# Performance work log

Measured on AMD Instinct MI355X. Metric: run time of the kernel, lower is better.

Reference implementation:

```python
import jax, jax.numpy as jnp
import numpy as np

B, F_IN, F_OUT, D, K = 32, 64, 64, 512, 64


def setup_inputs() -> dict:
    key = jax.random.key(0)
    k1, k2, k3 = jax.random.split(key, 3)
    x = jax.random.normal(k1, (B, F_IN, D), dtype=jnp.float32)
    # Evaluated monomial-word operators: K matrices of size D x D
    word_ops = jax.random.normal(k2, (K, D, D), dtype=jnp.float32)
    # nn.init.uniform_ -> U[0,1)
    coeff = jax.random.uniform(k3, (F_OUT, F_IN, K), dtype=jnp.float32)
    return {"x": x, "word_ops": word_ops, "coeff": coeff}


def reference(x, word_ops, coeff):
    # Per sample in the torch code:
    #   evals[i, d, k] = (X @ W_k)[i, d] = sum_e X[i, e] * W[k, e, d]
    #   res = tensordot(coeff, evals, ([1, 2], [0, 2]))  -> [F_out, D]
    # Fully batched fused contraction (replaces the Python loop over batch):
    # evals: [B, F_in, D, K]
    evals = jnp.einsum('bie,ked->bidk', x, word_ops)
    # out: [B, F_out, D]
    out = jnp.einsum('oik,bidk->bod', coeff, evals)
    return out
```

## Files before the change

kernel.cpp:

```cpp
#include <hip/hip_runtime.h>
#include <hip/hip_bf16.h>


#define KK 32768

typedef __attribute__((ext_vector_type(8))) short bf16x8;
typedef __attribute__((ext_vector_type(4))) float f32x4;

__device__ __forceinline__ unsigned short f2bf(float f) {
  unsigned int u = __float_as_uint(f);
  return (unsigned short)((u + 0x7FFFu + ((u >> 16) & 1u)) >> 16);
}

__device__ __forceinline__ unsigned int pkbf2(float a, float b) {
  __hip_bfloat162 h = __float22bfloat162_rn(make_float2(a, b));
  return *(unsigned int*)&h;
}

__device__ __forceinline__ void gld16(void* lds, const void* g) {
  __builtin_amdgcn_global_load_lds((const __attribute__((address_space(1))) void*)g,
                                   (__attribute__((address_space(3))) void*)lds,
                                   16, 0, 0);
}

__global__ __launch_bounds__(256) void convW(const float* __restrict__ W,
                                             unsigned short* __restrict__ WbT) {
  __shared__ float tile[64][65];
  int bx = blockIdx.x;
  int k = bx >> 6, et = (bx >> 3) & 7, dt = bx & 7;
  int t = threadIdx.x;
  const float* src = W + ((size_t)k * 512 + (size_t)et * 64) * 512 + dt * 64;
  int rr = t >> 6, cc = t & 63;
#pragma unroll
  for (int p = 0; p < 16; p++) {
    int e = p * 4 + rr;
    tile[e][cc] = src[(size_t)e * 512 + cc];
  }
  __syncthreads();
  int dl = t >> 4, eg = t & 15;
#pragma unroll
  for (int p = 0; p < 4; p++) {
    int d = p * 16 + dl;
    ushort4 v;
    v.x = f2bf(tile[eg * 4 + 0][d]);
    v.y = f2bf(tile[eg * 4 + 1][d]);
    v.z = f2bf(tile[eg * 4 + 2][d]);
    v.w = f2bf(tile[eg * 4 + 3][d]);
    *(ushort4*)(WbT + (size_t)(dt * 64 + d) * KK + k * 512 + et * 64 + eg * 4) = v;
  }
}

__global__ __launch_bounds__(256) void convXC(const float* __restrict__ x,
                                              const float* __restrict__ c,
                                              unsigned short* __restrict__ xT,
                                              unsigned short* __restrict__ cb) {
  __shared__ unsigned short lds[64 * 130];
  int t = threadIdx.x;
  if (blockIdx.x < 128) {
    int bx = blockIdx.x;
    int b = bx >> 2, ec = bx & 3;
    const float* src = x + (size_t)b * 32768 + ec * 128;
#pragma unroll
    for (int j = 0; j < 32; j++) {
      int idx = j * 256 + t;
      int i = idx >> 7, e = idx & 127;
      lds[i * 130 + e] = f2bf(src[(size_t)i * 512 + e]);
    }
    __syncthreads();
    unsigned short* dst = xT + (size_t)b * 32768 + ec * 128 * 64;
#pragma unroll
    for (int j = 0; j < 32; j++) {
      int idx = j * 256 + t;
      int e = idx >> 6, i = idx & 63;
      dst[idx] = lds[i * 130 + e];
    }
  } else {
    int rb = blockIdx.x - 128;
    const float* src = c + (size_t)rb * 4096;
#pragma unroll
    for (int j = 0; j < 16; j++) {
      int idx = j * 256 + t;
      int r = idx >> 6, k = idx & 63;
      lds[r * 66 + k] = f2bf(src[idx]);
    }
    __syncthreads();
#pragma unroll
    for (int j = 0; j < 16; j++) {
      int idx = j * 256 + t;
      int k = idx >> 6, r = idx & 63;
      cb[(size_t)k * 4096 + rb * 64 + r] = lds[r * 66 + k];
    }
  }
}

__global__ __launch_bounds__(256, 2) void fused_kern(const unsigned short* __restrict__ xT,
                                                     const unsigned short* __restrict__ cb,
                                                     const unsigned short* __restrict__ Bt,
                                                     float* __restrict__ out) {
  __shared__ unsigned short u[128 * 64];
  __shared__ unsigned short Bs[256 * 64];
  __shared__ unsigned short ck[4 * 64 * 64];
  int bx = blockIdx.x;
  int ks = bx & 15, np = (bx >> 4) & 1, mt = bx >> 5;
  int m0 = mt * 128, n0 = np * 256, kw0 = ks * 4, b0 = mt * 2;
  int t = threadIdx.x;
  int wid = t >> 6, lane = t & 63, q = lane >> 4, l16 = lane & 15;
  int wmb = wid & 1;
  int wnh = wid >> 1;
  int srow = t >> 3;
  int cg = (t & 7) ^ (srow & 7);
  {
    const unsigned short* gc = cb + (size_t)kw0 * 4096;
#pragma unroll
    for (int j = 0; j < 8; j++) {
      int row = j * 32 + srow;
      gld16((char*)ck + (j * 256 + t) * 16, gc + (size_t)row * 64 + cg * 8);
    }
  }
  f32x4 acc[4][8] = {};
#pragma unroll 1
  for (int ec = 0; ec < 8; ec++) {
#pragma unroll
    for (int j = 0; j < 4; j++) {
      int row = j * 32 + srow;
      int bl = row >> 6, el = row & 63;
      gld16((char*)u + (j * 256 + t) * 16,
            xT + (size_t)(b0 + bl) * 32768 + (size_t)(ec * 64 + el) * 64 + cg * 8);
    }
    __syncthreads();
    bf16x8 ax[4][2];
#pragma unroll
    for (int et = 0; et < 4; et++)
#pragma unroll
      for (int ks2 = 0; ks2 < 2; ks2++) {
        int row = wmb * 64 + et * 16 + l16;
        int s2 = (ks2 * 4 + q) ^ (row & 7);
        ax[et][ks2] = *(const bf16x8*)(u + row * 64 + s2 * 8);
      }
    __syncthreads();
#pragma unroll 1
    for (int k = 0; k < 4; k++) {
      const unsigned short* gb = Bt + (size_t)n0 * KK + (size_t)(kw0 + k) * 512 + ec * 64;
#pragma unroll
      for (int j = 0; j < 8; j++) {
        int row = j * 32 + srow;
        gld16((char*)Bs + (j * 256 + t) * 16, gb + (size_t)row * KK + cg * 8);
      }
      const unsigned short* ckk = ck + k * 4096;
      bf16x8 bc[2][2];
#pragma unroll
      for (int otl = 0; otl < 2; otl++)
#pragma unroll
        for (int ks2 = 0; ks2 < 2; ks2++) {
          int o = (wnh * 2 + otl) * 16 + l16;
          int s2 = (ks2 * 4 + q) ^ (o & 7);
          bc[otl][ks2] = *(const bf16x8*)(ckk + o * 64 + s2 * 8);
        }
      f32x4 td[4][2] = {};
#pragma unroll
      for (int et = 0; et < 4; et++)
#pragma unroll
        for (int otl = 0; otl < 2; otl++)
#pragma unroll
          for (int ks2 = 0; ks2 < 2; ks2++)
            td[et][otl] = __builtin_amdgcn_mfma_f32_16x16x32_bf16(ax[et][ks2], bc[otl][ks2],
                                                                  td[et][otl], 0, 0, 0);
#pragma unroll
      for (int et = 0; et < 4; et++)
#pragma unroll
        for (int otl = 0; otl < 2; otl++) {
          int row = wmb * 64 + (wnh * 2 + otl) * 16 + l16;
          int c0 = et * 16 + q * 4;
          int phys = ((c0 >> 3) ^ (row & 7)) * 8 + (c0 & 7);
          uint2 v;
          v.x = pkbf2(td[et][otl][0], td[et][otl][1]);
          v.y = pkbf2(td[et][otl][2], td[et][otl][3]);
          *(uint2*)(u + row * 64 + phys) = v;
        }
      __syncthreads();
#pragma unroll
      for (int ks2 = 0; ks2 < 2; ks2++) {
        bf16x8 af[4], bfr[8];
#pragma unroll
        for (int mf = 0; mf < 4; mf++) {
          int row = wmb * 64 + mf * 16 + l16;
          af[mf] = *(const bf16x8*)(u + row * 64 + (((ks2 * 4 + q) ^ (row & 7))) * 8);
        }
#pragma unroll
        for (int nf = 0; nf < 8; nf++) {
          int row = wnh * 128 + nf * 16 + l16;
          bfr[nf] = *(const bf16x8*)(Bs + row * 64 + (((ks2 * 4 + q) ^ (row & 7))) * 8);
        }
#pragma unroll
        for (int mf = 0; mf < 4; mf++)
#pragma unroll
          for (int nf = 0; nf < 8; nf++)
            acc[mf][nf] = __builtin_amdgcn_mfma_f32_16x16x32_bf16(af[mf], bfr[nf],
                                                                  acc[mf][nf], 0, 0, 0);
      }
      __syncthreads();
    }
  }
#pragma unroll
  for (int mf = 0; mf < 4; mf++)
#pragma unroll
    for (int nf = 0; nf < 8; nf++)
#pragma unroll
      for (int r = 0; r < 4; r++)
        atomicAdd(&out[(size_t)(m0 + wmb * 64 + mf * 16 + q * 4 + r) * 512
                       + n0 + wnh * 128 + nf * 16 + l16],
                  acc[mf][nf][r]);
}

__global__ __launch_bounds__(256) void fallback_kern(const float* __restrict__ x,
                                                     const float* __restrict__ W,
                                                     const float* __restrict__ coeff,
                                                     float* __restrict__ out) {
  __shared__ float ev[64][129];
  int b = blockIdx.x >> 6, k = blockIdx.x & 63;
  int t = threadIdx.x, dl = t & 127, half = t >> 7;
  const float* xb = x + (size_t)b * 64 * 512;
  const float* Wk = W + (size_t)k * 512 * 512;
  for (int dc = 0; dc < 4; dc++) {
    int d = dc * 128 + dl;
    for (int i = half * 32; i < half * 32 + 32; i++) {
      float acc = 0.f;
      const float* xr = xb + (size_t)i * 512;
#pragma unroll 4
      for (int e = 0; e < 512; e++) acc += xr[e] * Wk[(size_t)e * 512 + d];
      ev[i][dl] = acc;
    }
    __syncthreads();
    for (int o = half * 32; o < half * 32 + 32; o++) {
      float s = 0.f;
#pragma unroll 8
      for (int i = 0; i < 64; i++) s += coeff[((size_t)o * 64 + i) * 64 + k] * ev[i][dl];
      atomicAdd(&out[((size_t)(b * 64 + o)) * 512 + d], s);
    }
    __syncthreads();
  }
}

extern "C" void kernel_launch(void* const* d_in, const int* in_sizes, int n_in,
                              void* d_out, int out_size, void* d_ws, size_t ws_size,
                              hipStream_t stream) {
  const float* x = (const float*)d_in[0];
  const float* W = (const float*)d_in[1];
  const float* coeff = (const float*)d_in[2];
  float* out = (float*)d_out;
  const size_t OFF_XT = 33554432;
  const size_t OFF_CB = OFF_XT + 2097152;
  const size_t NEED = OFF_CB + 524288;

  hipMemsetAsync(d_out, 0, (size_t)out_size * sizeof(float), stream);
  if (ws_size >= NEED) {
    unsigned short* WbT = (unsigned short*)d_ws;
    unsigned short* xT  = (unsigned short*)((char*)d_ws + OFF_XT);
    unsigned short* cb  = (unsigned short*)((char*)d_ws + OFF_CB);
    convXC<<<192, 256, 0, stream>>>(x, coeff, xT, cb);
    convW<<<4096, 256, 0, stream>>>(W, WbT);
    fused_kern<<<512, 256, 0, stream>>>(xT, cb, WbT, out);
  } else {
    fallback_kern<<<2048, 256, 0, stream>>>(x, W, coeff, out);
  }
}
```

Before: 221.2 us.

## Merge N halves into 512-thread blocks with register-prefetched B pipeline

Each block now covers the full N=512 with 8 waves instead of two blocks per N-half, so the coefficient contraction (td) is computed once per block instead of twice. The k/ec loops are flattened into 32 stages. The next B tile is prefetched into registers and the next x chunk into a double-buffered LDS slot while the current stage computes. Waves use s_setprio around MFMA bursts. This uses more LDS and registers per block and halves the grid to 256 blocks, which may reduce occupancy on the 256-CU part.

Result: slower. 333.2 us (+50.6%).

```diff
diff --git a/kernel.cpp b/kernel.cpp
--- a/kernel.cpp
+++ b/kernel.cpp
@@ -93,112 +93,146 @@
   }
 }
 
-__global__ __launch_bounds__(256, 2) void fused_kern(const unsigned short* __restrict__ xT,
+__global__ __launch_bounds__(512, 2) void fused_kern(const unsigned short* __restrict__ xT,
                                                      const unsigned short* __restrict__ cb,
                                                      const unsigned short* __restrict__ Bt,
                                                      float* __restrict__ out) {
-  __shared__ unsigned short u[128 * 64];
-  __shared__ unsigned short Bs[256 * 64];
-  __shared__ unsigned short ck[4 * 64 * 64];
+  __shared__ unsigned short u2[2][8192];
+  __shared__ unsigned short As[8192];
+  __shared__ unsigned short ck[16384];
+  __shared__ unsigned short Bs[32768];
   int bx = blockIdx.x;
-  int ks = bx & 15, np = (bx >> 4) & 1, mt = bx >> 5;
-  int m0 = mt * 128, n0 = np * 256, kw0 = ks * 4, b0 = mt * 2;
+  int ks = bx & 15, mt = bx >> 4;
+  int m0 = mt * 128, kw0 = ks * 4, b0 = mt * 2;
   int t = threadIdx.x;
   int wid = t >> 6, lane = t & 63, q = lane >> 4, l16 = lane & 15;
-  int wmb = wid & 1;
-  int wnh = wid >> 1;
+  int wm = wid & 1;
+  int wn = wid >> 1;
   int srow = t >> 3;
-  int cg = (t & 7) ^ (srow & 7);
-  {
-    const unsigned short* gc = cb + (size_t)kw0 * 4096;
-#pragma unroll
-    for (int j = 0; j < 8; j++) {
-      int row = j * 32 + srow;
-      gld16((char*)ck + (j * 256 + t) * 16, gc + (size_t)row * 64 + cg * 8);
-    }
-  }
+  int sslot = t & 7;
+#pragma unroll
+  for (int j = 0; j < 4; j++) {
+    int row = j * 64 + srow;
+    int cg = sslot ^ (row & 7);
+    gld16((char*)ck + (j * 512 + t) * 16,
+          cb + (size_t)kw0 * 4096 + (size_t)row * 64 + cg * 8);
+  }
+#pragma unroll
+  for (int j = 0; j < 2; j++) {
+    int row = j * 64 + srow;
+    int cg = sslot ^ (row & 7);
+    int bl = row >> 6, el = row & 63;
+    gld16((char*)u2[0] + (j * 512 + t) * 16,
+          xT + (size_t)(b0 + bl) * 32768 + (size_t)el * 64 + cg * 8);
+  }
+  uint4 pf[8];
+#pragma unroll
+  for (int j = 0; j < 8; j++) {
+    int row = j * 64 + srow;
+    int cg = sslot ^ (row & 7);
+    pf[j] = *(const uint4*)(Bt + (size_t)row * KK + (size_t)kw0 * 512 + cg * 8);
+  }
+#pragma unroll
+  for (int j = 0; j < 8; j++)
+    *(uint4*)(Bs + (size_t)(j * 512 + t) * 8) = pf[j];
+  asm volatile("s_waitcnt vmcnt(0) lgkmcnt(0)" ::: "memory");
+  __builtin_amdgcn_s_barrier();
+
   f32x4 acc[4][8] = {};
+  bf16x8 ax[4][2];
 #pragma unroll 1
-  for (int ec = 0; ec < 8; ec++) {
-#pragma unroll
-    for (int j = 0; j < 4; j++) {
-      int row = j * 32 + srow;
-      int bl = row >> 6, el = row & 63;
-      gld16((char*)u + (j * 256 + t) * 16,
-            xT + (size_t)(b0 + bl) * 32768 + (size_t)(ec * 64 + el) * 64 + cg * 8);
-    }
-    __syncthreads();
-    bf16x8 ax[4][2];
-#pragma unroll
-    for (int et = 0; et < 4; et++)
-#pragma unroll
-      for (int ks2 = 0; ks2 < 2; ks2++) {
-        int row = wmb * 64 + et * 16 + l16;
-        int s2 = (ks2 * 4 + q) ^ (row & 7);
-        ax[et][ks2] = *(const bf16x8*)(u + row * 64 + s2 * 8);
-      }
-    __syncthreads();
-#pragma unroll 1
-    for (int k = 0; k < 4; k++) {
-      const unsigned short* gb = Bt + (size_t)n0 * KK + (size_t)(kw0 + k) * 512 + ec * 64;
+  for (int s = 0; s < 32; s++) {
+    int ec = s >> 2, kw = s & 3, ub = ec & 1;
+    if (s < 31) {
+      int sn = s + 1, ecn = sn >> 2, kwn = sn & 3;
+      size_t colb = (size_t)(kw0 + kwn) * 512 + (size_t)ecn * 64;
 #pragma unroll
       for (int j = 0; j < 8; j++) {
-        int row = j * 32 + srow;
-        gld16((char*)Bs + (j * 256 + t) * 16, gb + (size_t)row * KK + cg * 8);
-      }
-      const unsigned short* ckk = ck + k * 4096;
-      bf16x8 bc[2][2];
-#pragma unroll
-      for (int otl = 0; otl < 2; otl++)
-#pragma unroll
-        for (int ks2 = 0; ks2 < 2; ks2++) {
-          int o = (wnh * 2 + otl) * 16 + l16;
-          int s2 = (ks2 * 4 + q) ^ (o & 7);
-          bc[otl][ks2] = *(const bf16x8*)(ckk + o * 64 + s2 * 8);
+        int row = j * 64 + srow;
+        int cg = sslot ^ (row & 7);
+        pf[j] = *(const uint4*)(Bt + (size_t)row * KK + colb + cg * 8);
+      }
+      if (kw == 3) {
+#pragma unroll
+        for (int j = 0; j < 2; j++) {
+          int row = j * 64 + srow;
+          int cg = sslot ^ (row & 7);
+          int bl = row >> 6, el = row & 63;
+          gld16((char*)u2[ub ^ 1] + (j * 512 + t) * 16,
+                xT + (size_t)(b0 + bl) * 32768 + (size_t)((ec + 1) * 64 + el) * 64 + cg * 8);
         }
-      f32x4 td[4][2] = {};
+      }
+    }
+    if (kw == 0) {
 #pragma unroll
       for (int et = 0; et < 4; et++)
 #pragma unroll
-        for (int otl = 0; otl < 2; otl++)
-#pragma unroll
-          for (int ks2 = 0; ks2 < 2; ks2++)
-            td[et][otl] = __builtin_amdgcn_mfma_f32_16x16x32_bf16(ax[et][ks2], bc[otl][ks2],
-                                                                  td[et][otl], 0, 0, 0);
+        for (int k2 = 0; k2 < 2; k2++) {
+          int row = wm * 64 + et * 16 + l16;
+          int sz = (k2 * 4 + q) ^ (row & 7);
+          ax[et][k2] = *(const bf16x8*)(&u2[ub][row * 64 + sz * 8]);
+        }
+    }
+    {
+      const unsigned short* ckk = ck + kw * 4096;
+      bf16x8 bc[2];
+#pragma unroll
+      for (int k2 = 0; k2 < 2; k2++) {
+        int o = wn * 16 + l16;
+        int sz = (k2 * 4 + q) ^ (o & 7);
+        bc[k2] = *(const bf16x8*)(ckk + o * 64 + sz * 8);
+      }
+      f32x4 td[4] = {};
+      __builtin_amdgcn_s_setprio(1);
 #pragma unroll
       for (int et = 0; et < 4; et++)
 #pragma unroll
-        for (int otl = 0; otl < 2; otl++) {
-          int row = wmb * 64 + (wnh * 2 + otl) * 16 + l16;
-          int c0 = et * 16 + q * 4;
-          int phys = ((c0 >> 3) ^ (row & 7)) * 8 + (c0 & 7);
-          uint2 v;
-          v.x = pkbf2(td[et][otl][0], td[et][otl][1]);
-          v.y = pkbf2(td[et][otl][2], td[et][otl][3]);
-          *(uint2*)(u + row * 64 + phys) = v;
-        }
-      __syncthreads();
-#pragma unroll
-      for (int ks2 = 0; ks2 < 2; ks2++) {
-        bf16x8 af[4], bfr[8];
-#pragma unroll
-        for (int mf = 0; mf < 4; mf++) {
-          int row = wmb * 64 + mf * 16 + l16;
-          af[mf] = *(const bf16x8*)(u + row * 64 + (((ks2 * 4 + q) ^ (row & 7))) * 8);
-        }
-#pragma unroll
-        for (int nf = 0; nf < 8; nf++) {
-          int row = wnh * 128 + nf * 16 + l16;
-          bfr[nf] = *(const bf16x8*)(Bs + row * 64 + (((ks2 * 4 + q) ^ (row & 7))) * 8);
-        }
-#pragma unroll
-        for (int mf = 0; mf < 4; mf++)
-#pragma unroll
-          for (int nf = 0; nf < 8; nf++)
-            acc[mf][nf] = __builtin_amdgcn_mfma_f32_16x16x32_bf16(af[mf], bfr[nf],
-                                                                  acc[mf][nf], 0, 0, 0);
-      }
-      __syncthreads();
+        for (int k2 = 0; k2 < 2; k2++)
+          td[et] = __builtin_amdgcn_mfma_f32_16x16x32_bf16(ax[et][k2], bc[k2], td[et], 0, 0, 0);
+      __builtin_amdgcn_s_setprio(0);
+#pragma unroll
+      for (int et = 0; et < 4; et++) {
+        int row = wm * 64 + wn * 16 + l16;
+        int c0 = et * 16 + q * 4;
+        int phys = ((c0 >> 3) ^ (row & 7)) * 8 + (c0 & 7);
+        uint2 v;
+        v.x = pkbf2(td[et][0], td[et][1]);
+        v.y = pkbf2(td[et][2], td[et][3]);
+        *(uint2*)(As + row * 64 + phys) = v;
+      }
+    }
+    asm volatile("s_waitcnt lgkmcnt(0)" ::: "memory");
+    __builtin_amdgcn_sched_barrier(0);
+    __builtin_amdgcn_s_barrier();
+#pragma unroll
+    for (int k2 = 0; k2 < 2; k2++) {
+      bf16x8 af[4], bfr[8];
+#pragma unroll
+      for (int mf = 0; mf < 4; mf++) {
+        int row = wm * 64 + mf * 16 + l16;
+        af[mf] = *(const bf16x8*)(As + row * 64 + (((k2 * 4 + q) ^ (row & 7))) * 8);
+      }
+#pragma unroll
+      for (int nf = 0; nf < 8; nf++) {
+        int row = wn * 128 + nf * 16 + l16;
+        bfr[nf] = *(const bf16x8*)(Bs + row * 64 + (((k2 * 4 + q) ^ (row & 7))) * 8);
+      }
+      __builtin_amdgcn_s_setprio(1);
+#pragma unroll
+      for (int mf = 0; mf < 4; mf++)
+#pragma unroll
+        for (int nf = 0; nf < 8; nf++)
+          acc[mf][nf] = __builtin_amdgcn_mfma_f32_16x16x32_bf16(af[mf], bfr[nf],
+                                                                acc[mf][nf], 0, 0, 0);
+      __builtin_amdgcn_s_setprio(0);
+    }
+    if (s < 31) {
+      asm volatile("s_waitcnt vmcnt(0)" ::: "memory");
+      __builtin_amdgcn_sched_barrier(0);
+      __builtin_amdgcn_s_barrier();
+#pragma unroll
+      for (int j = 0; j < 8; j++)
+        *(uint4*)(Bs + (size_t)(j * 512 + t) * 8) = pf[j];
     }
   }
 #pragma unroll
@@ -207,8 +241,8 @@
     for (int nf = 0; nf < 8; nf++)
 #pragma unroll
       for (int r = 0; r < 4; r++)
-        atomicAdd(&out[(size_t)(m0 + wmb * 64 + mf * 16 + q * 4 + r) * 512
-                       + n0 + wnh * 128 + nf * 16 + l16],
+        atomicAdd(&out[(size_t)(m0 + wm * 64 + mf * 16 + q * 4 + r) * 512
+                       + wn * 128 + nf * 16 + l16],
                   acc[mf][nf][r]);
 }
 
@@ -259,7 +293,7 @@
     unsigned short* cb  = (unsigned short*)((char*)d_ws + OFF_CB);
     convXC<<<192, 256, 0, stream>>>(x, coeff, xT, cb);
     convW<<<4096, 256, 0, stream>>>(W, WbT);
-    fused_kern<<<512, 256, 0, stream>>>(xT, cb, WbT, out);
+    fused_kern<<<256, 512, 0, stream>>>(xT, cb, WbT, out);
   } else {
     fallback_kern<<<2048, 256, 0, stream>>>(x, W, coeff, out);
   }
```
